# Performance work log

Measured on AMD Instinct MI355X. Metric: run time of the kernel, lower is better.

The kernel has to match this reference:

```python
import jax, jax.numpy as jnp
import numpy as np
from jax import lax

KS = 3  # kernel_size


def setup_inputs() -> dict:
    key = jax.random.key(0)
    k1, k2, k3 = jax.random.split(key, 3)
    B, D, C_IN, F = 4, 96, 16, 16
    feat = jax.random.normal(k1, (B, D, D, D, C_IN), dtype=jnp.float32)
    index = jax.random.randint(k2, (B, D, D, D), 0, 2, dtype=jnp.int32)
    # glorot-style scale for w [c_in * ks^3, filters]
    fan_in = C_IN * KS ** 3
    w = jax.random.normal(k3, (fan_in, F), dtype=jnp.float32) * jnp.float32(np.sqrt(2.0 / (fan_in + F)))
    b = jnp.zeros((F,), dtype=jnp.float32)
    return {"feat": feat, "index": index, "w": w, "b": b}


def reference(feat, index, w, b):
    # SparseConv: for every voxel where index != 0, gather the ks^3 neighborhood
    # (out-of-bounds neighbors read as zero), flatten to [N, ks^3 * C_in],
    # matmul with w, add b, and scatter back (zeros elsewhere).
    # The meshgrid('ij') offset order followed by reshape([-1, ks^3 * C_in])
    # makes w row index = ((dx*ks + dy)*ks + dz)*C_in + c_in, i.e. exactly a
    # dense 3-D cross-correlation kernel w.reshape(ks, ks, ks, C_in, F) with
    # SAME zero padding; the scatter_nd equals masking the output by index != 0.
    c_in = feat.shape[-1]
    filters = w.shape[-1]
    w_conv = w.reshape(KS, KS, KS, c_in, filters)  # DHWIO
    out = lax.conv_general_dilated(
        feat, w_conv,
        window_strides=(1, 1, 1),
        padding="SAME",
        dimension_numbers=("NDHWC", "DHWIO", "NDHWC"),
    ) + b
    mask = (index != 0)[..., None]  # [B, X, Y, Z, 1]
    return jnp.where(mask, out, jnp.zeros((), dtype=out.dtype))
```

## Files before the change

kernel.cpp:

```cpp
#include <hip/hip_runtime.h>

#define DSZ 96
#define CIN 16
#define NF  16
#define BUFB 28800

typedef __attribute__((ext_vector_type(8))) short short8;
typedef __attribute__((ext_vector_type(4))) float f32x4;

union I4S8 { int4 i; short8 s; };

__global__ void pack_w(const float* __restrict__ w, short* __restrict__ wpack) {
  const int t = threadIdx.x >> 6;
  const int l = threadIdx.x & 63;
  const int tap = 2 * t + (l >> 5);
  const int cib = ((l >> 4) & 1) * 8;
  const int f = l & 15;
  short v[8];
#pragma unroll
  for (int j = 0; j < 8; ++j) {
    float x = (tap <= 26) ? w[(tap * 16 + cib + j) * 16 + f] : 0.0f;
    unsigned u = __float_as_uint(x);
    u = (u + 0x7FFFu + ((u >> 16) & 1u)) >> 16;
    v[j] = (short)u;
  }
  short8 s;
#pragma unroll
  for (int j = 0; j < 8; ++j) s[j] = v[j];
  reinterpret_cast<short8*>(wpack)[t * 64 + l] = s;
}

__global__ __launch_bounds__(512, 2) void conv_mfma_zp(
    const float* __restrict__ feat, const int* __restrict__ index,
    const float* __restrict__ bias, const short8* __restrict__ wpack,
    float* __restrict__ out) {
  __shared__ short smem[2 * 50 * 288];

  const int tid = threadIdx.x;
  const int lane = tid & 63;
  const int wid = tid >> 6;

  const int d = blockIdx.x;
  int L = (d & 7) * 192 + (d >> 3);
  const int yt = L % 32;  L /= 32;
  const int xt = L % 12;
  const int b  = L / 12;
  const int x0 = xt * 8, y0 = yt * 3;

  short8 bw[14];
#pragma unroll
  for (int t = 0; t < 14; ++t) bw[t] = wpack[t * 64 + lane];

  auto stage = [&](int z0, int bufoff) {
#pragma unroll
    for (int k = 0; k < 2; ++k) {
      const int i = tid + k * 512;
      if (i < 900) {
        const int col = i / 18;
        const int zp  = i - col * 18;
        const int colx = col / 5, coly = col - colx * 5;
        const int gx = x0 + colx - 1, gy = y0 + coly - 1, gz = z0 + zp - 1;
        const bool ok = ((unsigned)gx < (unsigned)DSZ) &
                        ((unsigned)gy < (unsigned)DSZ) &
                        ((unsigned)gz < (unsigned)DSZ);
        const long off = ok ? ((long)(((b * DSZ + gx) * DSZ + gy) * DSZ + gz) * CIN) : 0;
        const float4* p = reinterpret_cast<const float4*>(feat + off);
        float4 q0 = p[0], q1 = p[1], q2 = p[2], q3 = p[3];
        unsigned m0 = __builtin_amdgcn_perm(__float_as_uint(q0.y), __float_as_uint(q0.x), 0x07060302u);
        unsigned m1 = __builtin_amdgcn_perm(__float_as_uint(q0.w), __float_as_uint(q0.z), 0x07060302u);
        unsigned m2 = __builtin_amdgcn_perm(__float_as_uint(q1.y), __float_as_uint(q1.x), 0x07060302u);
        unsigned m3 = __builtin_amdgcn_perm(__float_as_uint(q1.w), __float_as_uint(q1.z), 0x07060302u);
        unsigned m4 = __builtin_amdgcn_perm(__float_as_uint(q2.y), __float_as_uint(q2.x), 0x07060302u);
        unsigned m5 = __builtin_amdgcn_perm(__float_as_uint(q2.w), __float_as_uint(q2.z), 0x07060302u);
        unsigned m6 = __builtin_amdgcn_perm(__float_as_uint(q3.y), __float_as_uint(q3.x), 0x07060302u);
        unsigned m7 = __builtin_amdgcn_perm(__float_as_uint(q3.w), __float_as_uint(q3.z), 0x07060302u);
        if (!ok) { m0 = m1 = m2 = m3 = m4 = m5 = m6 = m7 = 0u; }
        const int byte0 = bufoff + ((col * 576 + zp * 32) ^ ((zp & 4) << 2));
        *reinterpret_cast<int4*>((char*)smem + byte0)        = make_int4(m0, m1, m2, m3);
        *reinterpret_cast<int4*>((char*)smem + (byte0 ^ 16)) = make_int4(m4, m5, m6, m7);
      }
    }
  };

  const int cx = wid;
  const int tp = lane >> 5;
  int pre[3];
#pragma unroll
  for (int dz = 0; dz < 3; ++dz) {
    const int zp = (lane & 15) + dz;
    pre[dz] = (zp * 32 + (lane & 16)) ^ ((zp & 4) << 2);
  }
  int laddr[14];
#pragma unroll
  for (int t = 0; t < 14; ++t) {
    const int tapA = 2 * t;
    const int tapB = (2 * t + 1 <= 26) ? (2 * t + 1) : 26;
    const int aA = ((cx + tapA / 9) * 5 + (tapA / 3) % 3) * 576 + pre[tapA % 3];
    const int aB = ((cx + tapB / 9) * 5 + (tapB / 3) % 3) * 576 + pre[tapB % 3];
    laddr[t] = tp ? aB : aA;
  }

  const int fq = lane & 15, hq = lane >> 4;
  const float bf = bias[fq];
  const char* smb = (const char*)smem;
  const int rowbase = (b * DSZ + (x0 + cx)) * DSZ + y0;

  auto compute = [&](int z0, int bufoff) {
#pragma unroll
    for (int cy = 0; cy < 3; ++cy) {
      f32x4 acc0 = {0.f, 0.f, 0.f, 0.f};
      f32x4 acc1 = {0.f, 0.f, 0.f, 0.f};
#pragma unroll
      for (int t = 0; t < 14; ++t) {
        I4S8 u;
        u.i = *reinterpret_cast<const int4*>(smb + bufoff + laddr[t] + cy * 576);
        if (t & 1)
          acc1 = __builtin_amdgcn_mfma_f32_16x16x32_bf16(u.s, bw[t], acc1, 0, 0, 0);
        else
          acc0 = __builtin_amdgcn_mfma_f32_16x16x32_bf16(u.s, bw[t], acc0, 0, 0, 0);
      }
      const int vb = (rowbase + cy) * DSZ + z0 + hq * 4;
      const int4 iv = *reinterpret_cast<const int4*>(index + vb);
      float* op = out + (long)vb * NF + fq;
      op[0 * NF] = iv.x ? (acc0[0] + acc1[0] + bf) : 0.0f;
      op[1 * NF] = iv.y ? (acc0[1] + acc1[1] + bf) : 0.0f;
      op[2 * NF] = iv.z ? (acc0[2] + acc1[2] + bf) : 0.0f;
      op[3 * NF] = iv.w ? (acc0[3] + acc1[3] + bf) : 0.0f;
    }
  };

  stage(0, 0);
  __syncthreads();
#pragma unroll
  for (int zt = 0; zt < 6; ++zt) {
    if (zt < 5) stage((zt + 1) * 16, ((zt + 1) & 1) * BUFB);
    compute(zt * 16, (zt & 1) * BUFB);
    __syncthreads();
  }
}

__global__ __launch_bounds__(256) void sparse_conv_f32(
    const float* __restrict__ feat, const int* __restrict__ index,
    const float* __restrict__ w, const float* __restrict__ bias,
    float* __restrict__ out) {
  const int v = blockIdx.x * 256 + threadIdx.x;
  const int z = v % DSZ;
  int t = v / DSZ;
  const int y = t % DSZ; t /= DSZ;
  const int x = t % DSZ;
  const int bb = t / DSZ;
  float acc[NF];
#pragma unroll
  for (int f = 0; f < NF; ++f) acc[f] = bias[f];
  const bool active = (index[v] != 0);
#pragma unroll 1
  for (int kx = -1; kx <= 1; ++kx) {
    const int xx = x + kx;
    const bool okx = ((unsigned)xx < (unsigned)DSZ);
#pragma unroll 1
    for (int ky = -1; ky <= 1; ++ky) {
      const int yy = y + ky;
      const bool oky = okx && ((unsigned)yy < (unsigned)DSZ);
#pragma unroll 1
      for (int kz = -1; kz <= 1; ++kz) {
        const int zz = z + kz;
        const bool ok = oky && ((unsigned)zz < (unsigned)DSZ);
        const long long off = ((((long long)bb * DSZ + xx) * DSZ + yy) * DSZ + zz) * CIN;
        float4 q0, q1, q2, q3;
        if (ok) {
          const float4* fp = reinterpret_cast<const float4*>(feat + off);
          q0 = fp[0]; q1 = fp[1]; q2 = fp[2]; q3 = fp[3];
        } else {
          q0 = q1 = q2 = q3 = make_float4(0.f, 0.f, 0.f, 0.f);
        }
        const float fv[CIN] = {q0.x, q0.y, q0.z, q0.w, q1.x, q1.y, q1.z, q1.w,
                               q2.x, q2.y, q2.z, q2.w, q3.x, q3.y, q3.z, q3.w};
        const float* wr = w + ((((kx + 1) * 3 + (ky + 1)) * 3 + (kz + 1)) * CIN) * NF;
#pragma unroll
        for (int ci = 0; ci < CIN; ++ci) {
          const float fvv = fv[ci];
#pragma unroll
          for (int f = 0; f < NF; ++f) acc[f] = fmaf(fvv, wr[ci * NF + f], acc[f]);
        }
      }
    }
  }
  float4* op = reinterpret_cast<float4*>(out + (long long)v * NF);
  if (active) {
    op[0] = make_float4(acc[0], acc[1], acc[2], acc[3]);
    op[1] = make_float4(acc[4], acc[5], acc[6], acc[7]);
    op[2] = make_float4(acc[8], acc[9], acc[10], acc[11]);
    op[3] = make_float4(acc[12], acc[13], acc[14], acc[15]);
  } else {
    const float4 z4 = make_float4(0.f, 0.f, 0.f, 0.f);
    op[0] = z4; op[1] = z4; op[2] = z4; op[3] = z4;
  }
}

extern "C" void kernel_launch(void* const* d_in, const int* in_sizes, int n_in,
                              void* d_out, int out_size, void* d_ws, size_t ws_size,
                              hipStream_t stream) {
  const float* feat  = (const float*)d_in[0];
  const int*   index = (const int*)d_in[1];
  const float* w     = (const float*)d_in[2];
  const float* bias  = (const float*)d_in[3];
  float*       out   = (float*)d_out;

  const int nvox = in_sizes[1];

  if (ws_size < 14 * 64 * 8 * sizeof(short)) {
    sparse_conv_f32<<<nvox / 256, 256, 0, stream>>>(feat, index, w, bias, out);
    return;
  }

  short* wpack = (short*)d_ws;
  pack_w<<<1, 14 * 64, 0, stream>>>(w, wpack);

  const int blocks = 4 * 12 * 32;
  conv_mfma_zp<<<blocks, 512, 0, stream>>>(feat, index, bias,
                                           (const short8*)wpack, out);
}
```

Before: 144.0 us.

## Split block into producer and consumer waves for staging and MFMA compute

```diff
diff --git a/kernel.cpp b/kernel.cpp
--- a/kernel.cpp
+++ b/kernel.cpp
@@ -30,7 +30,7 @@
   reinterpret_cast<short8*>(wpack)[t * 64 + l] = s;
 }
 
-__global__ __launch_bounds__(512, 2) void conv_mfma_zp(
+__global__ __launch_bounds__(512, 2) void conv_mfma_pc(
     const float* __restrict__ feat, const int* __restrict__ index,
     const float* __restrict__ bias, const short8* __restrict__ wpack,
     float* __restrict__ out) {
@@ -47,95 +47,112 @@
   const int b  = L / 12;
   const int x0 = xt * 8, y0 = yt * 3;
 
-  short8 bw[14];
-#pragma unroll
-  for (int t = 0; t < 14; ++t) bw[t] = wpack[t * 64 + lane];
-
-  auto stage = [&](int z0, int bufoff) {
-#pragma unroll
-    for (int k = 0; k < 2; ++k) {
-      const int i = tid + k * 512;
-      if (i < 900) {
-        const int col = i / 18;
-        const int zp  = i - col * 18;
-        const int colx = col / 5, coly = col - colx * 5;
-        const int gx = x0 + colx - 1, gy = y0 + coly - 1, gz = z0 + zp - 1;
-        const bool ok = ((unsigned)gx < (unsigned)DSZ) &
-                        ((unsigned)gy < (unsigned)DSZ) &
-                        ((unsigned)gz < (unsigned)DSZ);
-        const long off = ok ? ((long)(((b * DSZ + gx) * DSZ + gy) * DSZ + gz) * CIN) : 0;
-        const float4* p = reinterpret_cast<const float4*>(feat + off);
-        float4 q0 = p[0], q1 = p[1], q2 = p[2], q3 = p[3];
-        unsigned m0 = __builtin_amdgcn_perm(__float_as_uint(q0.y), __float_as_uint(q0.x), 0x07060302u);
-        unsigned m1 = __builtin_amdgcn_perm(__float_as_uint(q0.w), __float_as_uint(q0.z), 0x07060302u);
-        unsigned m2 = __builtin_amdgcn_perm(__float_as_uint(q1.y), __float_as_uint(q1.x), 0x07060302u);
-        unsigned m3 = __builtin_amdgcn_perm(__float_as_uint(q1.w), __float_as_uint(q1.z), 0x07060302u);
-        unsigned m4 = __builtin_amdgcn_perm(__float_as_uint(q2.y), __float_as_uint(q2.x), 0x07060302u);
-        unsigned m5 = __builtin_amdgcn_perm(__float_as_uint(q2.w), __float_as_uint(q2.z), 0x07060302u);
-        unsigned m6 = __builtin_amdgcn_perm(__float_as_uint(q3.y), __float_as_uint(q3.x), 0x07060302u);
-        unsigned m7 = __builtin_amdgcn_perm(__float_as_uint(q3.w), __float_as_uint(q3.z), 0x07060302u);
-        if (!ok) { m0 = m1 = m2 = m3 = m4 = m5 = m6 = m7 = 0u; }
-        const int byte0 = bufoff + ((col * 576 + zp * 32) ^ ((zp & 4) << 2));
-        *reinterpret_cast<int4*>((char*)smem + byte0)        = make_int4(m0, m1, m2, m3);
-        *reinterpret_cast<int4*>((char*)smem + (byte0 ^ 16)) = make_int4(m4, m5, m6, m7);
+  if (wid >= 4) {
+    const int ptid = tid - 256;
+    auto stage = [&](int z0, int bufoff) {
+#pragma unroll
+      for (int k = 0; k < 4; ++k) {
+        const int i = ptid + k * 256;
+        if (i < 900) {
+          const int col = i / 18;
+          const int zp  = i - col * 18;
+          const int colx = col / 5, coly = col - colx * 5;
+          const int gx = x0 + colx - 1, gy = y0 + coly - 1, gz = z0 + zp - 1;
+          const bool ok = ((unsigned)gx < (unsigned)DSZ) &
+                          ((unsigned)gy < (unsigned)DSZ) &
+                          ((unsigned)gz < (unsigned)DSZ);
+          const long off = ok ? ((long)(((b * DSZ + gx) * DSZ + gy) * DSZ + gz) * CIN) : 0;
+          const float4* p = reinterpret_cast<const float4*>(feat + off);
+          float4 q0 = p[0], q1 = p[1], q2 = p[2], q3 = p[3];
+          unsigned m0 = __builtin_amdgcn_perm(__float_as_uint(q0.y), __float_as_uint(q0.x), 0x07060302u);
+          unsigned m1 = __builtin_amdgcn_perm(__float_as_uint(q0.w), __float_as_uint(q0.z), 0x07060302u);
+          unsigned m2 = __builtin_amdgcn_perm(__float_as_uint(q1.y), __float_as_uint(q1.x), 0x07060302u);
+          unsigned m3 = __builtin_amdgcn_perm(__float_as_uint(q1.w), __float_as_uint(q1.z), 0x07060302u);
+          unsigned m4 = __builtin_amdgcn_perm(__float_as_uint(q2.y), __float_as_uint(q2.x), 0x07060302u);
+          unsigned m5 = __builtin_amdgcn_perm(__float_as_uint(q2.w), __float_as_uint(q2.z), 0x07060302u);
+          unsigned m6 = __builtin_amdgcn_perm(__float_as_uint(q3.y), __float_as_uint(q3.x), 0x07060302u);
+          unsigned m7 = __builtin_amdgcn_perm(__float_as_uint(q3.w), __float_as_uint(q3.z), 0x07060302u);
+          if (!ok) { m0 = m1 = m2 = m3 = m4 = m5 = m6 = m7 = 0u; }
+          const int byte0 = bufoff + ((col * 576 + zp * 32) ^ ((zp & 4) << 2));
+          *reinterpret_cast<int4*>((char*)smem + byte0)        = make_int4(m0, m1, m2, m3);
+          *reinterpret_cast<int4*>((char*)smem + (byte0 ^ 16)) = make_int4(m4, m5, m6, m7);
+        }
       }
-    }
-  };
-
-  const int cx = wid;
-  const int tp = lane >> 5;
-  int pre[3];
-#pragma unroll
-  for (int dz = 0; dz < 3; ++dz) {
-    const int zp = (lane & 15) + dz;
-    pre[dz] = (zp * 32 + (lane & 16)) ^ ((zp & 4) << 2);
-  }
-  int laddr[14];
-#pragma unroll
-  for (int t = 0; t < 14; ++t) {
-    const int tapA = 2 * t;
-    const int tapB = (2 * t + 1 <= 26) ? (2 * t + 1) : 26;
-    const int aA = ((cx + tapA / 9) * 5 + (tapA / 3) % 3) * 576 + pre[tapA % 3];
-    const int aB = ((cx + tapB / 9) * 5 + (tapB / 3) % 3) * 576 + pre[tapB % 3];
-    laddr[t] = tp ? aB : aA;
-  }
-
-  const int fq = lane & 15, hq = lane >> 4;
-  const float bf = bias[fq];
-  const char* smb = (const char*)smem;
-  const int rowbase = (b * DSZ + (x0 + cx)) * DSZ + y0;
-
-  auto compute = [&](int z0, int bufoff) {
-#pragma unroll
-    for (int cy = 0; cy < 3; ++cy) {
-      f32x4 acc0 = {0.f, 0.f, 0.f, 0.f};
-      f32x4 acc1 = {0.f, 0.f, 0.f, 0.f};
-#pragma unroll
-      for (int t = 0; t < 14; ++t) {
-        I4S8 u;
-        u.i = *reinterpret_cast<const int4*>(smb + bufoff + laddr[t] + cy * 576);
-        if (t & 1)
-          acc1 = __builtin_amdgcn_mfma_f32_16x16x32_bf16(u.s, bw[t], acc1, 0, 0, 0);
-        else
-          acc0 = __builtin_amdgcn_mfma_f32_16x16x32_bf16(u.s, bw[t], acc0, 0, 0, 0);
+    };
+
+    stage(0, 0);
+    __syncthreads();
+#pragma unroll 1
+    for (int r = 0; r < 3; ++r) {
+      stage((2 * r + 1) * 16, BUFB);
+      __syncthreads();
+      if (r < 2) stage((2 * r + 2) * 16, 0);
+      __syncthreads();
+    }
+  } else {
+    short8 bw[14];
+#pragma unroll
+    for (int t = 0; t < 14; ++t) bw[t] = wpack[t * 64 + lane];
+
+    const int cx = 2 * wid;
+    const int tp = lane >> 5;
+    int pre[3];
+#pragma unroll
+    for (int dz = 0; dz < 3; ++dz) {
+      const int zp = (lane & 15) + dz;
+      pre[dz] = (zp * 32 + (lane & 16)) ^ ((zp & 4) << 2);
+    }
+    int laddr[14];
+#pragma unroll
+    for (int t = 0; t < 14; ++t) {
+      const int tapA = 2 * t;
+      const int tapB = (2 * t + 1 <= 26) ? (2 * t + 1) : 26;
+      const int aA = ((cx + tapA / 9) * 5 + (tapA / 3) % 3) * 576 + pre[tapA % 3];
+      const int aB = ((cx + tapB / 9) * 5 + (tapB / 3) % 3) * 576 + pre[tapB % 3];
+      laddr[t] = tp ? aB : aA;
+    }
+
+    const int fq = lane & 15, hq = lane >> 4;
+    const float bf = bias[fq];
+    const char* smb = (const char*)smem;
+    const int rowbase = (b * DSZ + (x0 + cx)) * DSZ + y0;
+
+    auto compute = [&](int z0, int bufconst) {
+#pragma unroll
+      for (int s = 0; s < 2; ++s) {
+        const int soff = s * 2880;
+#pragma unroll
+        for (int cy = 0; cy < 3; ++cy) {
+          f32x4 acc0 = {0.f, 0.f, 0.f, 0.f};
+          f32x4 acc1 = {0.f, 0.f, 0.f, 0.f};
+#pragma unroll
+          for (int t = 0; t < 14; ++t) {
+            I4S8 u;
+            u.i = *reinterpret_cast<const int4*>(smb + laddr[t] + (bufconst + soff + cy * 576));
+            if (t & 1)
+              acc1 = __builtin_amdgcn_mfma_f32_16x16x32_bf16(u.s, bw[t], acc1, 0, 0, 0);
+            else
+              acc0 = __builtin_amdgcn_mfma_f32_16x16x32_bf16(u.s, bw[t], acc0, 0, 0, 0);
+          }
+          const int vb = (rowbase + s * DSZ + cy) * DSZ + z0 + hq * 4;
+          const int4 iv = *reinterpret_cast<const int4*>(index + vb);
+          float* op = out + (long)vb * NF + fq;
+          op[0 * NF] = iv.x ? (acc0[0] + acc1[0] + bf) : 0.0f;
+          op[1 * NF] = iv.y ? (acc0[1] + acc1[1] + bf) : 0.0f;
+          op[2 * NF] = iv.z ? (acc0[2] + acc1[2] + bf) : 0.0f;
+          op[3 * NF] = iv.w ? (acc0[3] + acc1[3] + bf) : 0.0f;
+        }
       }
-      const int vb = (rowbase + cy) * DSZ + z0 + hq * 4;
-      const int4 iv = *reinterpret_cast<const int4*>(index + vb);
-      float* op = out + (long)vb * NF + fq;
-      op[0 * NF] = iv.x ? (acc0[0] + acc1[0] + bf) : 0.0f;
-      op[1 * NF] = iv.y ? (acc0[1] + acc1[1] + bf) : 0.0f;
-      op[2 * NF] = iv.z ? (acc0[2] + acc1[2] + bf) : 0.0f;
-      op[3 * NF] = iv.w ? (acc0[3] + acc1[3] + bf) : 0.0f;
-    }
-  };
-
-  stage(0, 0);
-  __syncthreads();
-#pragma unroll
-  for (int zt = 0; zt < 6; ++zt) {
-    if (zt < 5) stage((zt + 1) * 16, ((zt + 1) & 1) * BUFB);
-    compute(zt * 16, (zt & 1) * BUFB);
+    };
+
     __syncthreads();
+#pragma unroll 1
+    for (int r = 0; r < 3; ++r) {
+      compute((2 * r) * 16, 0);
+      __syncthreads();
+      compute((2 * r + 1) * 16, BUFB);
+      __syncthreads();
+    }
   }
 }
 
@@ -217,6 +234,6 @@
   pack_w<<<1, 14 * 64, 0, stream>>>(w, wpack);
 
   const int blocks = 4 * 12 * 32;
-  conv_mfma_zp<<<blocks, 512, 0, stream>>>(feat, index, bias,
+  conv_mfma_pc<<<blocks, 512, 0, stream>>>(feat, index, bias,
                                            (const short8*)wpack, out);
 }
```

New measurement: 156.9 us. 1.09x slower.

## Split staging into early global loads and late LDS writes around MFMA compute

Applied to the files above, without the earlier changes.

```diff
diff --git a/kernel.cpp b/kernel.cpp
--- a/kernel.cpp
+++ b/kernel.cpp
@@ -30,7 +30,7 @@
   reinterpret_cast<short8*>(wpack)[t * 64 + l] = s;
 }
 
-__global__ __launch_bounds__(512, 2) void conv_mfma_zp(
+__global__ __launch_bounds__(512, 2) void conv_mfma_pipe2(
     const float* __restrict__ feat, const int* __restrict__ index,
     const float* __restrict__ bias, const short8* __restrict__ wpack,
     float* __restrict__ out) {
@@ -51,36 +51,56 @@
 #pragma unroll
   for (int t = 0; t < 14; ++t) bw[t] = wpack[t * 64 + lane];
 
-  auto stage = [&](int z0, int bufoff) {
-#pragma unroll
-    for (int k = 0; k < 2; ++k) {
-      const int i = tid + k * 512;
-      if (i < 900) {
-        const int col = i / 18;
-        const int zp  = i - col * 18;
-        const int colx = col / 5, coly = col - colx * 5;
-        const int gx = x0 + colx - 1, gy = y0 + coly - 1, gz = z0 + zp - 1;
-        const bool ok = ((unsigned)gx < (unsigned)DSZ) &
-                        ((unsigned)gy < (unsigned)DSZ) &
-                        ((unsigned)gz < (unsigned)DSZ);
-        const long off = ok ? ((long)(((b * DSZ + gx) * DSZ + gy) * DSZ + gz) * CIN) : 0;
-        const float4* p = reinterpret_cast<const float4*>(feat + off);
-        float4 q0 = p[0], q1 = p[1], q2 = p[2], q3 = p[3];
-        unsigned m0 = __builtin_amdgcn_perm(__float_as_uint(q0.y), __float_as_uint(q0.x), 0x07060302u);
-        unsigned m1 = __builtin_amdgcn_perm(__float_as_uint(q0.w), __float_as_uint(q0.z), 0x07060302u);
-        unsigned m2 = __builtin_amdgcn_perm(__float_as_uint(q1.y), __float_as_uint(q1.x), 0x07060302u);
-        unsigned m3 = __builtin_amdgcn_perm(__float_as_uint(q1.w), __float_as_uint(q1.z), 0x07060302u);
-        unsigned m4 = __builtin_amdgcn_perm(__float_as_uint(q2.y), __float_as_uint(q2.x), 0x07060302u);
-        unsigned m5 = __builtin_amdgcn_perm(__float_as_uint(q2.w), __float_as_uint(q2.z), 0x07060302u);
-        unsigned m6 = __builtin_amdgcn_perm(__float_as_uint(q3.y), __float_as_uint(q3.x), 0x07060302u);
-        unsigned m7 = __builtin_amdgcn_perm(__float_as_uint(q3.w), __float_as_uint(q3.z), 0x07060302u);
-        if (!ok) { m0 = m1 = m2 = m3 = m4 = m5 = m6 = m7 = 0u; }
-        const int byte0 = bufoff + ((col * 576 + zp * 32) ^ ((zp & 4) << 2));
-        *reinterpret_cast<int4*>((char*)smem + byte0)        = make_int4(m0, m1, m2, m3);
-        *reinterpret_cast<int4*>((char*)smem + (byte0 ^ 16)) = make_int4(m4, m5, m6, m7);
-      }
-    }
-  };
+  const int colA = tid / 18,           zpA = tid - colA * 18;
+  const int iB   = tid + 512;
+  const bool hasB = (iB < 900);
+  const int iBc  = hasB ? iB : 0;
+  const int colB = iBc / 18,           zpB = iBc - colB * 18;
+  const int cAx = colA / 5, cAy = colA - cAx * 5;
+  const int cBx = colB / 5, cBy = colB - cBx * 5;
+  const int gxA = x0 + cAx - 1, gyA = y0 + cAy - 1;
+  const int gxB = x0 + cBx - 1, gyB = y0 + cBy - 1;
+  const bool okxyA = ((unsigned)gxA < (unsigned)DSZ) & ((unsigned)gyA < (unsigned)DSZ);
+  const bool okxyB = hasB & ((unsigned)gxB < (unsigned)DSZ) & ((unsigned)gyB < (unsigned)DSZ);
+  const long rowA = okxyA ? ((long)((b * DSZ + gxA) * DSZ + gyA) * DSZ) : 0;
+  const long rowB = okxyB ? ((long)((b * DSZ + gxB) * DSZ + gyB) * DSZ) : 0;
+  const int bytA = (colA * 576 + zpA * 32) ^ ((zpA & 4) << 2);
+  const int bytB = (colB * 576 + zpB * 32) ^ ((zpB & 4) << 2);
+
+  float4 qA0, qA1, qB0, qB1;
+  bool okA = false, okB = false;
+
+  auto stage_issue = [&](int z0) {
+    const int gzA = z0 + zpA - 1;
+    okA = okxyA & ((unsigned)gzA < (unsigned)DSZ);
+    const float4* pA = reinterpret_cast<const float4*>(
+        feat + (okA ? (rowA + gzA) * CIN : 0));
+    qA0 = pA[0];
+    qA1 = pA[1];
+    const int gzB = z0 + zpB - 1;
+    okB = okxyB & ((unsigned)gzB < (unsigned)DSZ);
+    const float4* pB = reinterpret_cast<const float4*>(
+        feat + (okB ? (rowB + gzB) * CIN : 0));
+    qB0 = pB[0];
+    qB1 = pB[1];
+  };
+
+  auto stage_write = [&](int bufoff) {
+    {
+      unsigned m0 = __builtin_amdgcn_perm(__float_as_uint(qA0.y), __float_as_uint(qA0.x), 0x07060302u);
+      unsigned m1 = __builtin_amdgcn_perm(__float_as_uint(qA0.w), __float_as_uint(qA0.z), 0x07060302u);
+      unsigned m2 = __builtin_amdgcn_perm(__float_as_uint(qA1.y), __float_as_uint(qA1.x), 0x07060302u);
+      unsigned m3 = __builtin_amdgcn_perm(__float_as_uint(qA1.w), __float_as_uint(qA1.z), 0x07060302u);
+      if (!okA) { m0 = m1 = m2 = m3 = 0u; }
+      *reinterpret_cast<int4*>((char*)smem + bufoff + bytA) = make_int4(m0, m1, m2, m3);
+    }
+  };
+  (void)stage_write;
+
+
+  const int fq = lane & 15, hq = lane >> 4;
+  const float bf = bias[fq];
+  const char* smb = (const char*)smem;
 
   const int cx = wid;
   const int tp = lane >> 5;
@@ -100,10 +120,57 @@
     laddr[t] = tp ? aB : aA;
   }
 
-  const int fq = lane & 15, hq = lane >> 4;
-  const float bf = bias[fq];
-  const char* smb = (const char*)smem;
   const int rowbase = (b * DSZ + (x0 + cx)) * DSZ + y0;
+  int4 iv[3];
+
+  auto load_iv = [&](int z0) {
+#pragma unroll
+    for (int cy = 0; cy < 3; ++cy)
+      iv[cy] = *reinterpret_cast<const int4*>(index + (rowbase + cy) * DSZ + z0 + hq * 4);
+  };
+
+  auto issueA = [&](int z0) {
+    const int gz = z0 + zpA - 1;
+    okA = okxyA & ((unsigned)gz < (unsigned)DSZ);
+    const float4* p = reinterpret_cast<const float4*>(
+        feat + (okA ? (rowA + gz) * CIN : 0));
+    qA0 = p[0]; qA1 = p[1]; qB0 = p[2]; qB1 = p[3];
+  };
+
+  auto writeA = [&](int bufoff) {
+    unsigned m0 = __builtin_amdgcn_perm(__float_as_uint(qA0.y), __float_as_uint(qA0.x), 0x07060302u);
+    unsigned m1 = __builtin_amdgcn_perm(__float_as_uint(qA0.w), __float_as_uint(qA0.z), 0x07060302u);
+    unsigned m2 = __builtin_amdgcn_perm(__float_as_uint(qA1.y), __float_as_uint(qA1.x), 0x07060302u);
+    unsigned m3 = __builtin_amdgcn_perm(__float_as_uint(qA1.w), __float_as_uint(qA1.z), 0x07060302u);
+    unsigned m4 = __builtin_amdgcn_perm(__float_as_uint(qB0.y), __float_as_uint(qB0.x), 0x07060302u);
+    unsigned m5 = __builtin_amdgcn_perm(__float_as_uint(qB0.w), __float_as_uint(qB0.z), 0x07060302u);
+    unsigned m6 = __builtin_amdgcn_perm(__float_as_uint(qB1.y), __float_as_uint(qB1.x), 0x07060302u);
+    unsigned m7 = __builtin_amdgcn_perm(__float_as_uint(qB1.w), __float_as_uint(qB1.z), 0x07060302u);
+    if (!okA) { m0 = m1 = m2 = m3 = m4 = m5 = m6 = m7 = 0u; }
+    *reinterpret_cast<int4*>((char*)smem + bufoff + bytA)        = make_int4(m0, m1, m2, m3);
+    *reinterpret_cast<int4*>((char*)smem + bufoff + (bytA ^ 16)) = make_int4(m4, m5, m6, m7);
+  };
+
+  auto stageB = [&](int z0, int bufoff) {
+    if (hasB) {
+      const int gz = z0 + zpB - 1;
+      const bool ok = okxyB & ((unsigned)gz < (unsigned)DSZ);
+      const float4* p = reinterpret_cast<const float4*>(
+          feat + (ok ? (rowB + gz) * CIN : 0));
+      float4 q0 = p[0], q1 = p[1], q2 = p[2], q3 = p[3];
+      unsigned m0 = __builtin_amdgcn_perm(__float_as_uint(q0.y), __float_as_uint(q0.x), 0x07060302u);
+      unsigned m1 = __builtin_amdgcn_perm(__float_as_uint(q0.w), __float_as_uint(q0.z), 0x07060302u);
+      unsigned m2 = __builtin_amdgcn_perm(__float_as_uint(q1.y), __float_as_uint(q1.x), 0x07060302u);
+      unsigned m3 = __builtin_amdgcn_perm(__float_as_uint(q1.w), __float_as_uint(q1.z), 0x07060302u);
+      unsigned m4 = __builtin_amdgcn_perm(__float_as_uint(q2.y), __float_as_uint(q2.x), 0x07060302u);
+      unsigned m5 = __builtin_amdgcn_perm(__float_as_uint(q2.w), __float_as_uint(q2.z), 0x07060302u);
+      unsigned m6 = __builtin_amdgcn_perm(__float_as_uint(q3.y), __float_as_uint(q3.x), 0x07060302u);
+      unsigned m7 = __builtin_amdgcn_perm(__float_as_uint(q3.w), __float_as_uint(q3.z), 0x07060302u);
+      if (!ok) { m0 = m1 = m2 = m3 = m4 = m5 = m6 = m7 = 0u; }
+      *reinterpret_cast<int4*>((char*)smem + bufoff + bytB)        = make_int4(m0, m1, m2, m3);
+      *reinterpret_cast<int4*>((char*)smem + bufoff + (bytB ^ 16)) = make_int4(m4, m5, m6, m7);
+    }
+  };
 
   auto compute = [&](int z0, int bufoff) {
 #pragma unroll
@@ -120,21 +187,31 @@
           acc0 = __builtin_amdgcn_mfma_f32_16x16x32_bf16(u.s, bw[t], acc0, 0, 0, 0);
       }
       const int vb = (rowbase + cy) * DSZ + z0 + hq * 4;
-      const int4 iv = *reinterpret_cast<const int4*>(index + vb);
       float* op = out + (long)vb * NF + fq;
-      op[0 * NF] = iv.x ? (acc0[0] + acc1[0] + bf) : 0.0f;
-      op[1 * NF] = iv.y ? (acc0[1] + acc1[1] + bf) : 0.0f;
-      op[2 * NF] = iv.z ? (acc0[2] + acc1[2] + bf) : 0.0f;
-      op[3 * NF] = iv.w ? (acc0[3] + acc1[3] + bf) : 0.0f;
-    }
-  };
-
-  stage(0, 0);
+      op[0 * NF] = iv[cy].x ? (acc0[0] + acc1[0] + bf) : 0.0f;
+      op[1 * NF] = iv[cy].y ? (acc0[1] + acc1[1] + bf) : 0.0f;
+      op[2 * NF] = iv[cy].z ? (acc0[2] + acc1[2] + bf) : 0.0f;
+      op[3 * NF] = iv[cy].w ? (acc0[3] + acc1[3] + bf) : 0.0f;
+    }
+  };
+
+  issueA(0);
+  writeA(0);
+  stageB(0, 0);
   __syncthreads();
+
 #pragma unroll
   for (int zt = 0; zt < 6; ++zt) {
-    if (zt < 5) stage((zt + 1) * 16, ((zt + 1) & 1) * BUFB);
-    compute(zt * 16, (zt & 1) * BUFB);
+    const int buf = (zt & 1) * BUFB;
+    const int nbuf = ((zt + 1) & 1) * BUFB;
+    load_iv(zt * 16);
+    if (zt < 5) issueA((zt + 1) * 16);
+    __builtin_amdgcn_sched_barrier(0);
+    compute(zt * 16, buf);
+    if (zt < 5) {
+      writeA(nbuf);
+      stageB((zt + 1) * 16, nbuf);
+    }
     __syncthreads();
   }
 }
@@ -217,6 +294,6 @@
   pack_w<<<1, 14 * 64, 0, stream>>>(w, wpack);
 
   const int blocks = 4 * 12 * 32;
-  conv_mfma_zp<<<blocks, 512, 0, stream>>>(feat, index, bias,
-                                           (const short8*)wpack, out);
-}
+  conv_mfma_pipe2<<<blocks, 512, 0, stream>>>(feat, index, bias,
+                                              (const short8*)wpack, out);
+}
```

Measured after the change: 138.4 us. 3.9% less time.
